# Kernel optimization log

Measured on AMD Instinct MI355X. Metric: run time of the kernel, lower is better.

The kernel has to match this reference:

```python
import jax, jax.numpy as jnp
import numpy as np

N = 100000   # node_num
D = 256      # enforce_dim
L = 3        # num_layer
E = 200000   # interactions in update batch
B = 50000    # query pairs
W_DECAY = 1e-06
P = 2 * L + 2          # stacked projections per pair
F = P * P              # pair_wise_feature_dim = 64


def setup_inputs() -> dict:
    key = jax.random.key(0)
    ks = jax.random.split(key, 12)
    std = 1.0 / np.sqrt(D)
    inp = {}
    # random projection tables (layer 0 is the random base; layers 1..L are accumulated state)
    inp['rp0'] = jax.random.normal(ks[0], (N, D), jnp.float32) * std
    inp['rp1'] = jax.random.normal(ks[1], (N, D), jnp.float32) * std
    inp['rp2'] = jax.random.normal(ks[2], (N, D), jnp.float32) * std
    inp['rp3'] = jax.random.normal(ks[3], (N, D), jnp.float32) * std
    # sorted interaction timestamps in [0, 1e6]; next_time = times[-1]
    inp['times'] = jnp.sort(jax.random.uniform(ks[4], (E,), jnp.float32) * 1e6)
    inp['now_time'] = jnp.zeros((1,), jnp.float32)
    # MLP: 64 -> 256 -> 64 (stored as [in, out])
    inp['w1'] = jax.random.normal(ks[5], (F, 4 * F), jnp.float32) * (1.0 / np.sqrt(F))
    inp['b1'] = jnp.zeros((4 * F,), jnp.float32)
    inp['w2'] = jax.random.normal(ks[6], (4 * F, F), jnp.float32) * (1.0 / np.sqrt(4 * F))
    inp['b2'] = jnp.zeros((F,), jnp.float32)
    inp['src_ids'] = jax.random.randint(ks[7], (E,), 0, N, jnp.int32)
    inp['dst_ids'] = jax.random.randint(ks[8], (E,), 0, N, jnp.int32)
    inp['q_src'] = jax.random.randint(ks[9], (B,), 0, N, jnp.int32)
    inp['q_dst'] = jax.random.randint(ks[10], (B,), 0, N, jnp.int32)
    return inp


def _update_and_pairwise(rp0, rp1, rp2, rp3, times, now_time, w1, b1, w2, b2,
                         src_ids, dst_ids, q_src, q_dst):
    next_time = times[-1]
    decay = jnp.exp(-W_DECAY * (next_time - now_time[0]))
    # decay accumulated tables: rp[i] *= decay**i for i >= 1
    rps = [rp0, rp1 * decay, rp2 * decay ** 2, rp3 * decay ** 3]
    tw = jnp.exp(-W_DECAY * (next_time - times))[:, None]   # [E,1]
    # update(): for each layer i (all using the pre-update rp[i-1]):
    #   rp[i][src] += rp[i-1][dst] * tw ; rp[i][dst] += rp[i-1][src] * tw
    new = [rps[0]]
    for i in range(1, L + 1):
        upd = rps[i].at[src_ids].add(rps[i - 1][dst_ids] * tw)
        upd = upd.at[dst_ids].add(rps[i - 1][src_ids] * tw)
        new.append(upd)
    # get_pair_wise_feature()
    src_proj = jnp.stack([r[q_src] for r in new], axis=1)   # [B, L+1, D]
    dst_proj = jnp.stack([r[q_dst] for r in new], axis=1)   # [B, L+1, D]
    proj = jnp.concatenate([src_proj, dst_proj], axis=1)    # [B, P, D]
    gram = jnp.einsum('bpd,bqd->bpq', proj, proj).reshape(proj.shape[0], -1)  # [B, F]
    feat = jnp.log1p(jnp.maximum(gram, 0.0))                # not_scale=False path
    h = jax.nn.relu(feat @ w1 + b1)
    return h @ w2 + b2                                      # [B, F]


def reference(rp0, rp1, rp2, rp3, times, now_time, w1, b1, w2, b2,
              src_ids, dst_ids, q_src, q_dst):
    return _update_and_pairwise(rp0, rp1, rp2, rp3, times, now_time,
                                w1, b1, w2, b2, src_ids, dst_ids, q_src, q_dst)
```

## Files before the change

kernel.cpp:

```cpp
#include <hip/hip_runtime.h>
#include <math.h>

#define D 256
#define WDECAY 1e-6f
#define CHUNK 1024
#define MLP_P 64


__global__ __launch_bounds__(256) void hist_kernel(
    const int* __restrict__ src, const int* __restrict__ dst, int E,
    int* __restrict__ cnt)
{
    int i = blockIdx.x * blockDim.x + threadIdx.x;
    if (i < 2 * E) {
        int n = (i < E) ? src[i] : dst[i - E];
        atomicAdd(&cnt[n], 1);
    }
}

__global__ __launch_bounds__(256) void scan_partial(
    const int* __restrict__ cnt, int N, int* __restrict__ bsum)
{
    __shared__ int sdata[256];
    int b = blockIdx.x, t = threadIdx.x;
    int base = b * CHUNK + 4 * t;
    int s = 0;
    if (base + 3 < N) {
        int4 v = *(const int4*)(cnt + base);
        s = v.x + v.y + v.z + v.w;
    } else {
        for (int k = 0; k < 4; ++k)
            if (base + k < N) s += cnt[base + k];
    }
    sdata[t] = s;
    __syncthreads();
    for (int off = 128; off > 0; off >>= 1) {
        if (t < off) sdata[t] += sdata[t + off];
        __syncthreads();
    }
    if (t == 0) bsum[b] = sdata[0];
}

__global__ __launch_bounds__(256) void scan_blocksums(
    int* __restrict__ bsum, int NB, int* __restrict__ row_start, int N)
{
    __shared__ int part[256];
    int t = threadIdx.x;
    int per = (NB + 255) / 256;
    int lo = t * per, hi = lo + per;
    if (hi > NB) hi = NB;
    int s = 0;
    for (int i = lo; i < hi; ++i) s += bsum[i];
    part[t] = s;
    __syncthreads();
    for (int off = 1; off < 256; off <<= 1) {
        int v = (t >= off) ? part[t - off] : 0;
        __syncthreads();
        part[t] += v;
        __syncthreads();
    }
    int base = (t == 0) ? 0 : part[t - 1];
    for (int i = lo; i < hi; ++i) {
        int c = bsum[i];
        bsum[i] = base;
        base += c;
    }
    if (t == 255) row_start[N] = part[255];
}

__global__ __launch_bounds__(256) void scan_apply(
    int* __restrict__ cnt, const int* __restrict__ bsum,
    int* __restrict__ row_start, int N)
{
    __shared__ int part[256];
    int b = blockIdx.x, t = threadIdx.x;
    int base = b * CHUNK + 4 * t;
    int4 v = make_int4(0, 0, 0, 0);
    if (base + 3 < N) {
        v = *(const int4*)(cnt + base);
    } else {
        if (base + 0 < N) v.x = cnt[base + 0];
        if (base + 1 < N) v.y = cnt[base + 1];
        if (base + 2 < N) v.z = cnt[base + 2];
    }
    part[t] = v.x + v.y + v.z + v.w;
    __syncthreads();
    for (int off = 1; off < 256; off <<= 1) {
        int pv = (t >= off) ? part[t - off] : 0;
        __syncthreads();
        part[t] += pv;
        __syncthreads();
    }
    int p = bsum[b] + ((t == 0) ? 0 : part[t - 1]);
    int p0 = p, p1 = p0 + v.x, p2 = p1 + v.y, p3 = p2 + v.z;
    if (base + 0 < N) { row_start[base + 0] = p0; cnt[base + 0] = p0; }
    if (base + 1 < N) { row_start[base + 1] = p1; cnt[base + 1] = p1; }
    if (base + 2 < N) { row_start[base + 2] = p2; cnt[base + 2] = p2; }
    if (base + 3 < N) { row_start[base + 3] = p3; cnt[base + 3] = p3; }
}

__global__ __launch_bounds__(256) void fill_kernel(
    const int* __restrict__ src, const int* __restrict__ dst,
    const float* __restrict__ times, int E,
    int* __restrict__ cursor, int* __restrict__ adj_other,
    float* __restrict__ adj_tw)
{
    int i = blockIdx.x * blockDim.x + threadIdx.x;
    if (i >= 2 * E) return;
    int e = (i < E) ? i : i - E;
    int node  = (i < E) ? src[e] : dst[e];
    int other = (i < E) ? dst[e] : src[e];
    float tlast = times[E - 1];
    float w = expf(-WDECAY * (tlast - times[e]));
    int pos = atomicAdd(&cursor[node], 1);
    adj_other[pos] = other;
    adj_tw[pos] = w;
}

__global__ __launch_bounds__(256) void set_flags(
    const int* __restrict__ qs, const int* __restrict__ qd, int B,
    int* __restrict__ flag)
{
    int i = blockIdx.x * blockDim.x + threadIdx.x;
    if (i < B) {
        flag[qs[i]] = 1;
        flag[qd[i]] = 1;
    }
}

__global__ __launch_bounds__(64) void apply_updates(
    const float* __restrict__ rp0, const float* __restrict__ rp1,
    const float* __restrict__ rp2, const float* __restrict__ rp3,
    const float* __restrict__ times, const float* __restrict__ now_time, int E,
    const int* __restrict__ row_start, const int* __restrict__ adj_other,
    const float* __restrict__ adj_tw, const int* __restrict__ flag,
    float* __restrict__ new1, float* __restrict__ new2, float* __restrict__ new3)
{
    int n = blockIdx.x;
    if (!flag[n]) return;
    int l = blockIdx.y;
    int lid = threadIdx.x;
    float tlast = times[E - 1];
    float dec = expf(-WDECAY * (tlast - now_time[0]));

    const float* own; const float* gat; float* outp; float os, gs;
    if (l == 0)      { own = rp1; gat = rp0; outp = new1; os = dec;             gs = 1.f;       }
    else if (l == 1) { own = rp2; gat = rp1; outp = new2; os = dec * dec;       gs = dec;       }
    else             { own = rp3; gat = rp2; outp = new3; os = dec * dec * dec; gs = dec * dec; }

    long long base = (long long)n * D + lid * 4;
    float4 acc = *(const float4*)(own + base);
    acc.x *= os; acc.y *= os; acc.z *= os; acc.w *= os;

    int s = row_start[n];
    int e = row_start[n + 1];
    for (int j = s; j < e; ++j) {
        int o = adj_other[j];
        float w = adj_tw[j] * gs;
        float4 v = *(const float4*)(gat + (long long)o * D + lid * 4);
        acc.x += v.x * w; acc.y += v.y * w; acc.z += v.z * w; acc.w += v.w * w;
    }
    *(float4*)(outp + base) = acc;
}


__global__ __launch_bounds__(64) void gather_gram(
    const float* __restrict__ rp0, const float* __restrict__ new1,
    const float* __restrict__ new2, const float* __restrict__ new3,
    const int* __restrict__ q_src, const int* __restrict__ q_dst,
    float* __restrict__ featT, int B)
{
    __shared__ float proj[8][260];
    int b = blockIdx.x;
    int lid = threadIdx.x;
    long long qs = q_src[b];
    long long qd = q_dst[b];

    const float* tabs[4] = {rp0, new1, new2, new3};
    #pragma unroll
    for (int r = 0; r < 4; ++r) {
        const float* tp = tabs[r];
        float4 v = *(const float4*)(tp + qs * D + lid * 4);
        *(float4*)&proj[r][lid * 4] = v;
        float4 w = *(const float4*)(tp + qd * D + lid * 4);
        *(float4*)&proj[r + 4][lid * 4] = w;
    }
    __syncthreads();

    int p = lid >> 3;
    int q = lid & 7;
    float acc = 0.f;
    #pragma unroll 8
    for (int k = 0; k < 64; ++k) {
        float4 a = *(const float4*)&proj[p][4 * k];
        float4 c = *(const float4*)&proj[q][4 * k];
        acc += a.x * c.x + a.y * c.y + a.z * c.z + a.w * c.w;
    }
    featT[(long long)lid * B + b] = log1pf(fmaxf(acc, 0.f));
}

__global__ __launch_bounds__(256, 1) void mlp_kernel(
    const float* __restrict__ featT,
    const float* __restrict__ w1,
    const float* __restrict__ b1,
    const float* __restrict__ w2,
    const float* __restrict__ b2,
    float* __restrict__ out, int B)
{
    __shared__ float fsT[64][68];
    __shared__ float hT[256][65];
    int t = threadIdx.x;
    int p0 = blockIdx.x * MLP_P;

    {
        int p = t & 63;
        int gp = p0 + p;
        bool valid = (gp < B);
        #pragma unroll
        for (int r = 0; r < 16; ++r) {
            int k = (t >> 6) + 4 * r;
            fsT[k][p] = valid ? featT[(long long)k * B + gp] : 0.f;
        }
    }
    __syncthreads();

    {
        int tp = t >> 5;
        int to = t & 31;
        float acc[8][8];
        #pragma unroll
        for (int i = 0; i < 8; ++i)
            #pragma unroll
            for (int j = 0; j < 8; ++j) acc[i][j] = 0.f;

        #pragma unroll 4
        for (int k = 0; k < 64; ++k) {
            float4 fA = *(const float4*)&fsT[k][tp * 8];
            float4 fB = *(const float4*)&fsT[k][tp * 8 + 4];
            const float* wr = w1 + k * 256 + to;
            float w[8];
            #pragma unroll
            for (int j = 0; j < 8; ++j) w[j] = wr[32 * j];
            float f0 = fA.x, f1 = fA.y, f2 = fA.z, f3 = fA.w;
            float f4 = fB.x, f5 = fB.y, f6 = fB.z, f7 = fB.w;
            #pragma unroll
            for (int j = 0; j < 8; ++j) {
                acc[0][j] += f0 * w[j]; acc[1][j] += f1 * w[j];
                acc[2][j] += f2 * w[j]; acc[3][j] += f3 * w[j];
                acc[4][j] += f4 * w[j]; acc[5][j] += f5 * w[j];
                acc[6][j] += f6 * w[j]; acc[7][j] += f7 * w[j];
            }
        }
        #pragma unroll
        for (int j = 0; j < 8; ++j) {
            int o = to + 32 * j;
            float bb = b1[o];
            #pragma unroll
            for (int i = 0; i < 8; ++i)
                hT[o][tp * 8 + i] = fmaxf(acc[i][j] + bb, 0.f);
        }
    }
    __syncthreads();

    {
        int tp2 = t >> 4;
        int tc  = t & 15;
        float a0x = 0.f, a0y = 0.f, a0z = 0.f, a0w = 0.f;
        float a1x = 0.f, a1y = 0.f, a1z = 0.f, a1w = 0.f;
        float a2x = 0.f, a2y = 0.f, a2z = 0.f, a2w = 0.f;
        float a3x = 0.f, a3y = 0.f, a3z = 0.f, a3w = 0.f;

        #pragma unroll 4
        for (int k = 0; k < 256; ++k) {
            float h0 = hT[k][tp2 * 4 + 0];
            float h1 = hT[k][tp2 * 4 + 1];
            float h2 = hT[k][tp2 * 4 + 2];
            float h3 = hT[k][tp2 * 4 + 3];
            float4 wv = *(const float4*)&w2[k * 64 + tc * 4];
            a0x += h0 * wv.x; a0y += h0 * wv.y; a0z += h0 * wv.z; a0w += h0 * wv.w;
            a1x += h1 * wv.x; a1y += h1 * wv.y; a1z += h1 * wv.z; a1w += h1 * wv.w;
            a2x += h2 * wv.x; a2y += h2 * wv.y; a2z += h2 * wv.z; a2w += h2 * wv.w;
            a3x += h3 * wv.x; a3y += h3 * wv.y; a3z += h3 * wv.z; a3w += h3 * wv.w;
        }
        float4 bv = *(const float4*)&b2[tc * 4];
        int gp = p0 + tp2 * 4;
        float* op = out + (long long)gp * 64 + tc * 4;
        if (gp + 0 < B) *(float4*)(op + 0 * 64) =
            make_float4(a0x + bv.x, a0y + bv.y, a0z + bv.z, a0w + bv.w);
        if (gp + 1 < B) *(float4*)(op + 1 * 64) =
            make_float4(a1x + bv.x, a1y + bv.y, a1z + bv.z, a1w + bv.w);
        if (gp + 2 < B) *(float4*)(op + 2 * 64) =
            make_float4(a2x + bv.x, a2y + bv.y, a2z + bv.z, a2w + bv.w);
        if (gp + 3 < B) *(float4*)(op + 3 * 64) =
            make_float4(a3x + bv.x, a3y + bv.y, a3z + bv.z, a3w + bv.w);
    }
}


__global__ __launch_bounds__(256) void init_tables(
    const float* __restrict__ rp1, const float* __restrict__ rp2,
    const float* __restrict__ rp3, const float* __restrict__ times,
    const float* __restrict__ now_time, int E,
    float* __restrict__ new1, float* __restrict__ new2, float* __restrict__ new3,
    long long n4)
{
    float tlast = times[E - 1];
    float dec = expf(-WDECAY * (tlast - now_time[0]));
    float d2 = dec * dec;
    float d3 = d2 * dec;
    const float4* r1 = (const float4*)rp1;
    const float4* r2 = (const float4*)rp2;
    const float4* r3 = (const float4*)rp3;
    float4* n1 = (float4*)new1;
    float4* n2 = (float4*)new2;
    float4* n3 = (float4*)new3;
    long long i = (long long)blockIdx.x * blockDim.x + threadIdx.x;
    long long stride = (long long)gridDim.x * blockDim.x;
    for (; i < n4; i += stride) {
        float4 a = r1[i]; a.x *= dec; a.y *= dec; a.z *= dec; a.w *= dec; n1[i] = a;
        float4 b = r2[i]; b.x *= d2; b.y *= d2; b.z *= d2; b.w *= d2; n2[i] = b;
        float4 c = r3[i]; c.x *= d3; c.y *= d3; c.z *= d3; c.w *= d3; n3[i] = c;
    }
}

__global__ __launch_bounds__(256) void scatter_edges(
    const float* __restrict__ rp0, const float* __restrict__ rp1,
    const float* __restrict__ rp2, const float* __restrict__ times,
    const float* __restrict__ now_time,
    const int* __restrict__ src_ids, const int* __restrict__ dst_ids, int E,
    float* __restrict__ new1, float* __restrict__ new2, float* __restrict__ new3)
{
    int e = blockIdx.x;
    int d = threadIdx.x;
    float tlast = times[E - 1];
    float dec = expf(-WDECAY * (tlast - now_time[0]));
    float d2 = dec * dec;
    float tw = expf(-WDECAY * (tlast - times[e]));
    long long s = src_ids[e];
    long long t = dst_ids[e];
    long long so = s * D + d;
    long long to = t * D + d;
    float a0s = rp0[so], a0t = rp0[to];
    atomicAdd(&new1[so], a0t * tw);
    atomicAdd(&new1[to], a0s * tw);
    float a1s = rp1[so] * dec, a1t = rp1[to] * dec;
    atomicAdd(&new2[so], a1t * tw);
    atomicAdd(&new2[to], a1s * tw);
    float a2s = rp2[so] * d2, a2t = rp2[to] * d2;
    atomicAdd(&new3[so], a2t * tw);
    atomicAdd(&new3[to], a2s * tw);
}

__global__ __launch_bounds__(64) void pair_feature_mlp(
    const float* __restrict__ rp0, const float* __restrict__ new1,
    const float* __restrict__ new2, const float* __restrict__ new3,
    const int* __restrict__ q_src, const int* __restrict__ q_dst,
    const float* __restrict__ w1, const float* __restrict__ b1,
    const float* __restrict__ w2, const float* __restrict__ b2,
    float* __restrict__ out, int B)
{
    __shared__ float proj[8][260];
    __shared__ float feat_s[64];
    __shared__ float h_s[256];

    int b = blockIdx.x;
    int lid = threadIdx.x;
    long long qs = q_src[b];
    long long qd = q_dst[b];

    const float* tabs[4] = {rp0, new1, new2, new3};
    #pragma unroll
    for (int r = 0; r < 4; ++r) {
        const float* tp = tabs[r];
        float4 v = *(const float4*)(tp + qs * D + lid * 4);
        *(float4*)&proj[r][lid * 4] = v;
        float4 w = *(const float4*)(tp + qd * D + lid * 4);
        *(float4*)&proj[r + 4][lid * 4] = w;
    }
    __syncthreads();

    int p = lid >> 3;
    int q = lid & 7;
    float acc = 0.f;
    #pragma unroll 8
    for (int k = 0; k < 64; ++k) {
        float4 a = *(const float4*)&proj[p][4 * k];
        float4 c = *(const float4*)&proj[q][4 * k];
        acc += a.x * c.x + a.y * c.y + a.z * c.z + a.w * c.w;
    }
    feat_s[lid] = log1pf(fmaxf(acc, 0.f));
    __syncthreads();

    float4 hv = *(const float4*)(b1 + 4 * lid);
    #pragma unroll 4
    for (int i = 0; i < 64; ++i) {
        float fv = feat_s[i];
        float4 w = *(const float4*)(w1 + i * 256 + 4 * lid);
        hv.x += fv * w.x; hv.y += fv * w.y; hv.z += fv * w.z; hv.w += fv * w.w;
    }
    *(float4*)&h_s[4 * lid] = make_float4(fmaxf(hv.x, 0.f), fmaxf(hv.y, 0.f),
                                          fmaxf(hv.z, 0.f), fmaxf(hv.w, 0.f));
    __syncthreads();

    float o0 = 0.f, o1 = 0.f, o2 = 0.f, o3 = 0.f;
    #pragma unroll 4
    for (int j = 0; j < 256; j += 4) {
        o0 += h_s[j + 0] * w2[(j + 0) * 64 + lid];
        o1 += h_s[j + 1] * w2[(j + 1) * 64 + lid];
        o2 += h_s[j + 2] * w2[(j + 2) * 64 + lid];
        o3 += h_s[j + 3] * w2[(j + 3) * 64 + lid];
    }
    out[(long long)b * 64 + lid] = b2[lid] + (o0 + o1) + (o2 + o3);
}

extern "C" void kernel_launch(void* const* d_in, const int* in_sizes, int n_in,
                              void* d_out, int out_size, void* d_ws, size_t ws_size,
                              hipStream_t stream)
{
    const float* rp0      = (const float*)d_in[0];
    const float* rp1      = (const float*)d_in[1];
    const float* rp2      = (const float*)d_in[2];
    const float* rp3      = (const float*)d_in[3];
    const float* times    = (const float*)d_in[4];
    const float* now_time = (const float*)d_in[5];
    const float* w1       = (const float*)d_in[6];
    const float* b1       = (const float*)d_in[7];
    const float* w2       = (const float*)d_in[8];
    const float* b2       = (const float*)d_in[9];
    const int*   src_ids  = (const int*)d_in[10];
    const int*   dst_ids  = (const int*)d_in[11];
    const int*   q_src    = (const int*)d_in[12];
    const int*   q_dst    = (const int*)d_in[13];
    float* out = (float*)d_out;

    long long ND = in_sizes[0];
    int N = (int)(ND / D);
    int E = in_sizes[4];
    int B = in_sizes[12];
    int NB = (N + CHUNK - 1) / CHUNK;

    float* new1 = (float*)d_ws;
    float* new2 = new1 + ND;
    float* new3 = new2 + ND;

    size_t base_bytes = (size_t)3 * ND * sizeof(float);
    size_t extra_bytes = (size_t)(2 * N + (N + 1) + 2 * E + NB) * sizeof(int)
                       + (size_t)(2 * E) * sizeof(float)
                       + (size_t)B * 64 * sizeof(float);

    if (ws_size >= base_bytes + extra_bytes && NB <= 65536) {
        int* cnt       = (int*)(new3 + ND);
        int* flag      = cnt + N;
        int* row_start = flag + N;
        int* adj_other = row_start + N + 1;
        float* adj_tw  = (float*)(adj_other + 2 * E);
        int* bsum      = (int*)(adj_tw + 2 * E);
        float* featT   = (float*)(bsum + NB);

        hipMemsetAsync(cnt, 0, (size_t)2 * N * sizeof(int), stream);
        int twoE = 2 * E;
        hist_kernel<<<(twoE + 255) / 256, 256, 0, stream>>>(src_ids, dst_ids, E, cnt);
        set_flags<<<(B + 255) / 256, 256, 0, stream>>>(q_src, q_dst, B, flag);
        scan_partial<<<NB, 256, 0, stream>>>(cnt, N, bsum);
        scan_blocksums<<<1, 256, 0, stream>>>(bsum, NB, row_start, N);
        scan_apply<<<NB, 256, 0, stream>>>(cnt, bsum, row_start, N);
        fill_kernel<<<(twoE + 255) / 256, 256, 0, stream>>>(src_ids, dst_ids, times, E,
                                                            cnt, adj_other, adj_tw);
        dim3 grid(N, 3);
        apply_updates<<<grid, 64, 0, stream>>>(rp0, rp1, rp2, rp3, times, now_time, E,
                                               row_start, adj_other, adj_tw, flag,
                                               new1, new2, new3);
        gather_gram<<<B, 64, 0, stream>>>(rp0, new1, new2, new3, q_src, q_dst, featT, B);
        mlp_kernel<<<(B + MLP_P - 1) / MLP_P, 256, 0, stream>>>(featT, w1, b1, w2, b2,
                                                                out, B);
    } else {
        long long n4 = ND / 4;
        init_tables<<<2048, 256, 0, stream>>>(rp1, rp2, rp3, times, now_time, E,
                                              new1, new2, new3, n4);
        scatter_edges<<<E, 256, 0, stream>>>(rp0, rp1, rp2, times, now_time,
                                             src_ids, dst_ids, E, new1, new2, new3);
        pair_feature_mlp<<<B, 64, 0, stream>>>(rp0, new1, new2, new3, q_src, q_dst,
                                               w1, b1, w2, b2, out, B);
    }
}
```

Baseline: 682.2 us.

## Split MLP into two kernels with staged weights and row-major features

Gram features are now written row-major instead of transposed. The single fused MLP kernel is split into two kernels. The first computes the hidden layer with W1 staged in shared memory and writes H to global memory. The second reads H to produce the output. Smaller per-block tiles and a two-blocks-per-CU launch bound aim to raise occupancy over the LDS-heavy fused kernel, at the cost of a B×256 float round trip through global memory. The split path runs only when the workspace is large enough; otherwise a fused kernel, also modified to stage W1 in LDS, is used.

```diff
diff --git a/kernel.cpp b/kernel.cpp
--- a/kernel.cpp
+++ b/kernel.cpp
@@ -5,6 +5,8 @@
 #define WDECAY 1e-6f
 #define CHUNK 1024
 #define MLP_P 64
+#define P1 32
+#define P2 32
 
 
 __global__ __launch_bounds__(256) void hist_kernel(
@@ -168,7 +170,7 @@
     const float* __restrict__ rp0, const float* __restrict__ new1,
     const float* __restrict__ new2, const float* __restrict__ new3,
     const int* __restrict__ q_src, const int* __restrict__ q_dst,
-    float* __restrict__ featT, int B)
+    float* __restrict__ feat, int B)
 {
     __shared__ float proj[8][260];
     int b = blockIdx.x;
@@ -196,11 +198,127 @@
         float4 c = *(const float4*)&proj[q][4 * k];
         acc += a.x * c.x + a.y * c.y + a.z * c.z + a.w * c.w;
     }
-    featT[(long long)lid * B + b] = log1pf(fmaxf(acc, 0.f));
-}
-
-__global__ __launch_bounds__(256, 1) void mlp_kernel(
-    const float* __restrict__ featT,
+    feat[(long long)b * 64 + lid] = log1pf(fmaxf(acc, 0.f));
+}
+
+__global__ __launch_bounds__(256, 2) void mlp1_kernel(
+    const float* __restrict__ feat,
+    const float* __restrict__ w1,
+    const float* __restrict__ b1,
+    float* __restrict__ H,
+    int B)
+{
+    __shared__ float w1s[64][256];
+    __shared__ float fsT[64][36];
+    int t = threadIdx.x;
+    int p0 = blockIdx.x * P1;
+
+    {
+        const float4* wg = (const float4*)w1;
+        float4* wd = (float4*)&w1s[0][0];
+        #pragma unroll
+        for (int r = 0; r < 16; ++r) wd[t + 256 * r] = wg[t + 256 * r];
+    }
+    #pragma unroll
+    for (int r = 0; r < 8; ++r) {
+        int idx = t + 256 * r;
+        int p = idx >> 6;
+        int k = idx & 63;
+        int gp = p0 + p;
+        fsT[k][p] = (gp < B) ? feat[(long long)gp * 64 + k] : 0.f;
+    }
+    __syncthreads();
+
+    int tp = t >> 6;
+    int to = t & 63;
+    float4 acc[8];
+    #pragma unroll
+    for (int i = 0; i < 8; ++i) acc[i] = make_float4(0.f, 0.f, 0.f, 0.f);
+
+    #pragma unroll 4
+    for (int k = 0; k < 64; ++k) {
+        float4 fA = *(const float4*)&fsT[k][tp * 8];
+        float4 fB = *(const float4*)&fsT[k][tp * 8 + 4];
+        float4 wv = *(const float4*)&w1s[k][to * 4];
+        float f_[8] = {fA.x, fA.y, fA.z, fA.w, fB.x, fB.y, fB.z, fB.w};
+        #pragma unroll
+        for (int i = 0; i < 8; ++i) {
+            acc[i].x += f_[i] * wv.x; acc[i].y += f_[i] * wv.y;
+            acc[i].z += f_[i] * wv.z; acc[i].w += f_[i] * wv.w;
+        }
+    }
+
+    float4 bv = *(const float4*)&b1[to * 4];
+    #pragma unroll
+    for (int i = 0; i < 8; ++i) {
+        int gp = p0 + tp * 8 + i;
+        if (gp < B) {
+            float4 h = make_float4(fmaxf(acc[i].x + bv.x, 0.f),
+                                   fmaxf(acc[i].y + bv.y, 0.f),
+                                   fmaxf(acc[i].z + bv.z, 0.f),
+                                   fmaxf(acc[i].w + bv.w, 0.f));
+            *(float4*)&H[(long long)gp * 256 + to * 4] = h;
+        }
+    }
+}
+
+__global__ __launch_bounds__(256, 2) void mlp2_kernel(
+    const float* __restrict__ H,
+    const float* __restrict__ w2,
+    const float* __restrict__ b2,
+    float* __restrict__ out, int B)
+{
+    __shared__ float Hs[P2][260];
+    int t = threadIdx.x;
+    int p0 = blockIdx.x * P2;
+
+    #pragma unroll
+    for (int r = 0; r < 8; ++r) {
+        int idx = t + 256 * r;
+        int p = idx >> 6;
+        int k4 = idx & 63;
+        int gp = p0 + p;
+        float4 v = (gp < B) ? *(const float4*)&H[(long long)gp * 256 + k4 * 4]
+                            : make_float4(0.f, 0.f, 0.f, 0.f);
+        *(float4*)&Hs[p][k4 * 4] = v;
+    }
+    __syncthreads();
+
+    int tp2 = t >> 4;
+    int tc  = t & 15;
+    float4 a0 = make_float4(0.f, 0.f, 0.f, 0.f);
+    float4 a1 = make_float4(0.f, 0.f, 0.f, 0.f);
+
+    #pragma unroll 2
+    for (int k = 0; k < 256; k += 4) {
+        float4 h0 = *(const float4*)&Hs[tp2 * 2 + 0][k];
+        float4 h1 = *(const float4*)&Hs[tp2 * 2 + 1][k];
+        float4 w0 = *(const float4*)&w2[(k + 0) * 64 + tc * 4];
+        float4 w1v = *(const float4*)&w2[(k + 1) * 64 + tc * 4];
+        float4 w2v = *(const float4*)&w2[(k + 2) * 64 + tc * 4];
+        float4 w3 = *(const float4*)&w2[(k + 3) * 64 + tc * 4];
+        a0.x += h0.x * w0.x + h0.y * w1v.x + h0.z * w2v.x + h0.w * w3.x;
+        a0.y += h0.x * w0.y + h0.y * w1v.y + h0.z * w2v.y + h0.w * w3.y;
+        a0.z += h0.x * w0.z + h0.y * w1v.z + h0.z * w2v.z + h0.w * w3.z;
+        a0.w += h0.x * w0.w + h0.y * w1v.w + h0.z * w2v.w + h0.w * w3.w;
+        a1.x += h1.x * w0.x + h1.y * w1v.x + h1.z * w2v.x + h1.w * w3.x;
+        a1.y += h1.x * w0.y + h1.y * w1v.y + h1.z * w2v.y + h1.w * w3.y;
+        a1.z += h1.x * w0.z + h1.y * w1v.z + h1.z * w2v.z + h1.w * w3.z;
+        a1.w += h1.x * w0.w + h1.y * w1v.w + h1.z * w2v.w + h1.w * w3.w;
+    }
+
+    float4 bv = *(const float4*)&b2[tc * 4];
+    int gp0 = p0 + tp2 * 2;
+    if (gp0 < B)
+        *(float4*)&out[(long long)gp0 * 64 + tc * 4] =
+            make_float4(a0.x + bv.x, a0.y + bv.y, a0.z + bv.z, a0.w + bv.w);
+    if (gp0 + 1 < B)
+        *(float4*)&out[(long long)(gp0 + 1) * 64 + tc * 4] =
+            make_float4(a1.x + bv.x, a1.y + bv.y, a1.z + bv.z, a1.w + bv.w);
+}
+
+__global__ __launch_bounds__(256, 1) void mlp_fused(
+    const float* __restrict__ feat,
     const float* __restrict__ w1,
     const float* __restrict__ b1,
     const float* __restrict__ w2,
@@ -208,19 +326,24 @@
     float* __restrict__ out, int B)
 {
     __shared__ float fsT[64][68];
+    __shared__ float w1s[64 * 256];
     __shared__ float hT[256][65];
     int t = threadIdx.x;
     int p0 = blockIdx.x * MLP_P;
 
     {
-        int p = t & 63;
+        const float4* wg = (const float4*)w1;
+        float4* wd = (float4*)w1s;
+        #pragma unroll
+        for (int r = 0; r < 16; ++r) wd[t + 256 * r] = wg[t + 256 * r];
+    }
+    #pragma unroll
+    for (int r = 0; r < 16; ++r) {
+        int idx = t + 256 * r;
+        int p = idx >> 6;
+        int k = idx & 63;
         int gp = p0 + p;
-        bool valid = (gp < B);
-        #pragma unroll
-        for (int r = 0; r < 16; ++r) {
-            int k = (t >> 6) + 4 * r;
-            fsT[k][p] = valid ? featT[(long long)k * B + gp] : 0.f;
-        }
+        fsT[k][p] = (gp < B) ? feat[(long long)gp * 64 + k] : 0.f;
     }
     __syncthreads();
 
@@ -237,7 +360,7 @@
         for (int k = 0; k < 64; ++k) {
             float4 fA = *(const float4*)&fsT[k][tp * 8];
             float4 fB = *(const float4*)&fsT[k][tp * 8 + 4];
-            const float* wr = w1 + k * 256 + to;
+            const float* wr = w1s + k * 256 + to;
             float w[8];
             #pragma unroll
             for (int j = 0; j < 8; ++j) w[j] = wr[32 * j];
@@ -270,7 +393,7 @@
         float a2x = 0.f, a2y = 0.f, a2z = 0.f, a2w = 0.f;
         float a3x = 0.f, a3y = 0.f, a3z = 0.f, a3w = 0.f;
 
-        #pragma unroll 4
+        #pragma unroll 8
         for (int k = 0; k < 256; ++k) {
             float h0 = hT[k][tp2 * 4 + 0];
             float h1 = hT[k][tp2 * 4 + 1];
@@ -444,18 +567,21 @@
     float* new3 = new2 + ND;
 
     size_t base_bytes = (size_t)3 * ND * sizeof(float);
-    size_t extra_bytes = (size_t)(2 * N + (N + 1) + 2 * E + NB) * sizeof(int)
-                       + (size_t)(2 * E) * sizeof(float)
-                       + (size_t)B * 64 * sizeof(float);
-
-    if (ws_size >= base_bytes + extra_bytes && NB <= 65536) {
+    size_t csr_bytes  = (size_t)(2 * N + (N + 1) + 2 * E + NB) * sizeof(int)
+                      + (size_t)(2 * E) * sizeof(float)
+                      + (size_t)B * 64 * sizeof(float);
+    size_t h_bytes    = (size_t)B * 256 * sizeof(float);
+
+    if (ws_size >= base_bytes + csr_bytes && NB <= 65536) {
         int* cnt       = (int*)(new3 + ND);
         int* flag      = cnt + N;
         int* row_start = flag + N;
         int* adj_other = row_start + N + 1;
         float* adj_tw  = (float*)(adj_other + 2 * E);
         int* bsum      = (int*)(adj_tw + 2 * E);
-        float* featT   = (float*)(bsum + NB);
+        float* feat    = (float*)(bsum + NB);
+        float* Hbuf    = feat + (size_t)B * 64;
+        bool   split   = (ws_size >= base_bytes + csr_bytes + h_bytes);
 
         hipMemsetAsync(cnt, 0, (size_t)2 * N * sizeof(int), stream);
         int twoE = 2 * E;
@@ -470,9 +596,14 @@
         apply_updates<<<grid, 64, 0, stream>>>(rp0, rp1, rp2, rp3, times, now_time, E,
                                                row_start, adj_other, adj_tw, flag,
                                                new1, new2, new3);
-        gather_gram<<<B, 64, 0, stream>>>(rp0, new1, new2, new3, q_src, q_dst, featT, B);
-        mlp_kernel<<<(B + MLP_P - 1) / MLP_P, 256, 0, stream>>>(featT, w1, b1, w2, b2,
-                                                                out, B);
+        gather_gram<<<B, 64, 0, stream>>>(rp0, new1, new2, new3, q_src, q_dst, feat, B);
+        if (split) {
+            mlp1_kernel<<<(B + P1 - 1) / P1, 256, 0, stream>>>(feat, w1, b1, Hbuf, B);
+            mlp2_kernel<<<(B + P2 - 1) / P2, 256, 0, stream>>>(Hbuf, w2, b2, out, B);
+        } else {
+            mlp_fused<<<(B + MLP_P - 1) / MLP_P, 256, 0, stream>>>(feat, w1, b1, w2, b2,
+                                                                   out, B);
+        }
     } else {
         long long n4 = ND / 4;
         init_tables<<<2048, 256, 0, stream>>>(rp1, rp2, rp3, times, now_time, E,
```

New measurement: 643.4 us. 5.7% less time.
